# Kernel optimization log

Hardware: AMD Instinct MI355X
Metric: run time of the kernel (lower is better)

Reference implementation:

```python
import jax, jax.numpy as jnp
import numpy as np
from jax import lax

B, DIM, H, W = 32, 256, 64, 64
DS = DIM // 4          # dim_split = 64
MLP_H = int(DIM * 2.0)  # mlp_ratio = 2.0
AK = 11                 # att_kernel
EPS = 1e-5


def conv(x, w, b=None, padding=(0, 0), dilation=1, groups=1, stride=1):
    y = lax.conv_general_dilated(
        x, w, (stride, stride),
        [(padding[0], padding[0]), (padding[1], padding[1])],
        rhs_dilation=(dilation, dilation),
        dimension_numbers=('NCHW', 'OIHW', 'NCHW'),
        feature_group_count=groups)
    if b is not None:
        y = y + b[None, :, None, None]
    return y


def bn(x):
    # BatchNorm2d, training-mode batch stats, affine at default init (gamma=1, beta=0)
    m = x.mean(axis=(0, 2, 3), keepdims=True)
    v = ((x - m) ** 2).mean(axis=(0, 2, 3), keepdims=True)
    return (x - m) * lax.rsqrt(v + EPS)


def maxpool2x2(x):
    b, c, h, w = x.shape
    xw = x.reshape(b, c, h // 2, 2, w // 2, 2).transpose(0, 1, 2, 4, 3, 5).reshape(b, c, h // 2, w // 2, 4)
    return xw.max(axis=-1), jnp.argmax(xw, axis=-1)


def maxunpool2x2(y, idx):
    b, c, h, w = y.shape
    oh = jax.nn.one_hot(idx, 4, dtype=y.dtype)  # scatter back into 2x2 window argmax slot
    out = (y[..., None] * oh).reshape(b, c, h, w, 2, 2).transpose(0, 1, 2, 4, 3, 5)
    return out.reshape(b, c, 2 * h, 2 * w)


def maxpool3(x):
    return lax.reduce_window(x, -jnp.inf, lax.max, (1, 1, 3, 3), (1, 1, 1, 1),
                             [(0, 0), (0, 0), (1, 1), (1, 1)])


def blurpool(x):
    # antialiased_cnns.BlurPool(C, stride=3): filt_size=4, reflect pad (1,2)
    f = jnp.array([1., 3., 3., 1.], dtype=x.dtype)
    k = f[:, None] * f[None, :]
    k = k / k.sum()
    c = x.shape[1]
    wgt = jnp.broadcast_to(k[None, None], (c, 1, 4, 4))
    xp = jnp.pad(x, ((0, 0), (0, 0), (1, 2), (1, 2)), mode='reflect')
    return lax.conv_general_dilated(xp, wgt, (3, 3), [(0, 0), (0, 0)],
                                    dimension_numbers=('NCHW', 'OIHW', 'NCHW'),
                                    feature_group_count=c)


def h_tf(x):
    b, c, hh, ww = x.shape
    x = jnp.pad(x, ((0, 0), (0, 0), (0, 0), (0, ww)))
    x = x.reshape(b, c, -1)[..., :-ww]
    return x.reshape(b, c, hh, 2 * ww - 1)


def inv_h_tf(x):
    b, c, hh, _ = x.shape
    x = x.reshape(b, c, -1)
    x = jnp.pad(x, ((0, 0), (0, 0), (0, hh)))
    return x.reshape(b, c, hh, 2 * hh)[..., :hh]


def v_tf(x):
    return h_tf(x.transpose(0, 1, 3, 2)).transpose(0, 1, 3, 2)


def inv_v_tf(x):
    return inv_h_tf(x.transpose(0, 1, 3, 2)).transpose(0, 1, 3, 2)


def ga12(x, p1w, p1b, c0w, c0b, spw, spb, c1w, c1b, c2w, c2b, cw, cb, sqw, sqb, p2w, p2b):
    xp, idx = maxpool2x2(x)
    c = xp.shape[1]
    h = jax.nn.relu(conv(xp, p1w, p1b))
    a1 = conv(h, c0w, c0b, padding=(2, 2), groups=c)                 # depthwise 5x5
    a2 = conv(a1, spw, spb, padding=(9, 9), dilation=3, groups=c)    # depthwise 7x7 dil3
    a1s = conv(a1, c1w, c1b)
    a2s = conv(a2, c2w, c2b)
    comb = jnp.concatenate([a1s, a2s], axis=1)
    agg = jnp.concatenate([comb.mean(axis=1, keepdims=True),
                           comb.max(axis=1, keepdims=True)], axis=1)
    sig = jax.nn.sigmoid(conv(agg, sqw, sqb, padding=(3, 3)))
    attn = conv(a1s * sig[:, 0:1] + a2s * sig[:, 1:2], cw, cb)
    h = conv(h * attn, p2w, p2b)
    return maxunpool2x2(h, idx)


def setup_inputs() -> dict:
    key = jax.random.key(0)
    ks = jax.random.split(key, 32)
    r = lambda i, shape: jax.random.normal(ks[i], shape, jnp.float32) * 0.05
    return {
        'x': jax.random.normal(ks[0], (B, DIM, H, W), jnp.float32),
        'pa_w1': r(1, (4 * DS, DS, 1, 1)),
        'pa_w2': r(2, (DS, 4 * DS, 1, 1)),
        'la_w': r(3, (DS, DS, 3, 3)),
        'mra_h1': r(4, (DS, 1, AK, 3)),
        'mra_v1': r(5, (DS, 1, 3, AK)),
        'mra_h2': r(6, (DS, 1, AK, 3)),
        'mra_v2': r(7, (DS, 1, 3, AK)),
        'g_proj1_w': r(8, (DS, DS, 1, 1)), 'g_proj1_b': r(9, (DS,)),
        'g_conv0_w': r(10, (DS, 1, 5, 5)), 'g_conv0_b': r(11, (DS,)),
        'g_sp_w': r(12, (DS, 1, 7, 7)), 'g_sp_b': r(13, (DS,)),
        'g_c1_w': r(14, (DS // 2, DS, 1, 1)), 'g_c1_b': r(15, (DS // 2,)),
        'g_c2_w': r(16, (DS // 2, DS, 1, 1)), 'g_c2_b': r(17, (DS // 2,)),
        'g_c_w': r(18, (DS, DS // 2, 1, 1)), 'g_c_b': r(19, (DS,)),
        'g_sq_w': r(20, (2, 2, 7, 7)), 'g_sq_b': r(21, (2,)),
        'g_proj2_w': r(22, (DS, DS, 1, 1)), 'g_proj2_b': r(23, (DS,)),
        'mlp_w1': r(24, (MLP_H, DIM, 1, 1)),
        'mlp_w2': r(25, (DIM, MLP_H, 1, 1)),
    }


def reference(x, pa_w1, pa_w2, la_w, mra_h1, mra_v1, mra_h2, mra_v2,
              g_proj1_w, g_proj1_b, g_conv0_w, g_conv0_b, g_sp_w, g_sp_b,
              g_c1_w, g_c1_b, g_c2_w, g_c2_b, g_c_w, g_c_b,
              g_sq_w, g_sq_b, g_proj2_w, g_proj2_b, mlp_w1, mlp_w2):
    x1, x2, x3, x4 = jnp.split(x, 4, axis=1)
    # PA: pixel attention (1x1 expand -> BN -> ReLU -> 1x1) sigmoid gate
    xa1 = x1 * jax.nn.sigmoid(conv(jax.nn.relu(bn(conv(x1, pa_w1))), pa_w2))
    # LA: 3x3 conv -> BN -> ReLU
    xa2 = jax.nn.relu(bn(conv(x2, la_w, padding=(1, 1))))
    # MRA: maxpool3x3 -> blurpool(stride3) -> 4 strip depthwise convs (+diag shear) -> BN -> sigmoid -> nearest upsample gate
    xm = blurpool(maxpool3(x3))
    ph, pv = (AK // 2, 1), (1, AK // 2)
    xh1 = conv(xm, mra_h1, padding=ph, groups=DS)
    xw1 = conv(xm, mra_v1, padding=pv, groups=DS)
    xh2 = inv_h_tf(conv(h_tf(xm), mra_h2, padding=ph, groups=DS))
    xw2 = inv_v_tf(conv(v_tf(xm), mra_v2, padding=pv, groups=DS))
    gate = jax.nn.sigmoid(bn(xh1 + xw1 + xh2 + xw2))
    hs, ws = gate.shape[-2:]
    ri = (jnp.arange(H) * hs) // H   # torch F.interpolate mode='nearest' index rule
    ci = (jnp.arange(W) * ws) // W
    xa3 = x3 * gate[:, :, ri][:, :, :, ci]
    # D_GA (stage==2): maxpool -> GA12 -> BN -> maxunpool
    x4p, idx1 = maxpool2x2(x4)
    xg = ga12(x4p, g_proj1_w, g_proj1_b, g_conv0_w, g_conv0_b, g_sp_w, g_sp_b,
              g_c1_w, g_c1_b, g_c2_w, g_c2_b, g_c_w, g_c_b, g_sq_w, g_sq_b,
              g_proj2_w, g_proj2_b)
    xa4 = maxunpool2x2(bn(xg), idx1)
    x_att = jnp.concatenate([xa1, xa2, xa3, xa4], axis=1)
    # residual MLP (drop_path=0 -> identity)
    return x + conv(jax.nn.relu(bn(conv(x_att, mlp_w1))), mlp_w2)
```

## Files before the change

### kernel.cpp

```cpp
#include <hip/hip_runtime.h>
#include <hip/hip_bf16.h>
#include <math.h>

typedef __hip_bfloat16 bf16;
typedef __attribute__((ext_vector_type(4))) float f32x4;
typedef __attribute__((ext_vector_type(8))) short s16x8;
typedef __attribute__((ext_vector_type(4))) short s16x4;

static __device__ __forceinline__ float bits2f(short s){ return __uint_as_float(((unsigned)(unsigned short)s)<<16); }
static __device__ __forceinline__ short bfbits(float f){ bf16 h = __float2bfloat16(f); return *reinterpret_cast<short*>(&h); }
static __device__ __forceinline__ float ldf(float v){ return v; }
static __device__ __forceinline__ float sigm(float v){ return 1.f/(1.f+__expf(-v)); }

#define P_IMG 4096

#define GLDS16(SRC, DST) __builtin_amdgcn_global_load_lds( \
    (__attribute__((address_space(1))) void*)(SRC), \
    (__attribute__((address_space(3))) void*)(DST), 16, 0, 0)

namespace {
constexpr long long XATT_OFF = 0;
constexpr long long BIG_OFF  = 67108864;
constexpr long long MISC     = 134217728;
constexpr long long XM_OFF   = MISC;
constexpr long long MSUM_OFF = MISC + 3964928;
constexpr long long SH_OFF   = MISC + 7929856;
constexpr long long SH2_OFF  = MISC + 15679488;
constexpr long long X4P_OFF  = MISC + 23429120;
constexpr long long IDX1_OFF = MISC + 31817728;
constexpr long long XP_OFF   = MISC + 40206336;
constexpr long long IDX2_OFF = MISC + 42303488;
constexpr long long HBUF_OFF = MISC + 44400640;
constexpr long long A1_OFF   = MISC + 46497792;
constexpr long long A2_OFF   = MISC + 48594944;
constexpr long long A1S_OFF  = MISC + 50692096;
constexpr long long A2S_OFF  = MISC + 51740672;
constexpr long long AGG_OFF  = MISC + 52789248;
constexpr long long SIG_OFF  = MISC + 52854784;
constexpr long long ATTN_OFF = MISC + 52920320;
constexpr long long H2_OFF   = MISC + 55017472;
constexpr long long XG_OFF   = MISC + 57114624;
constexpr long long P33_OFF  = 201326592;
constexpr long long STATS_OFF= 234881024;
constexpr long long WS_NEED  = 234897408;
constexpr long long XPM_OFF  = MISC;
constexpr long long YLA_OFF  = MISC + 33554432;
}

__global__ __launch_bounds__(256) void zero_out_k(float* __restrict__ o, int n){
    int i = blockIdx.x*256 + threadIdx.x;
    if (i < n) o[i] = 0.f;
}

__global__ __launch_bounds__(256) void packw_k(const float* __restrict__ W, short* __restrict__ Wp,
                                               int kshift, int OT16)
{
    int i = blockIdx.x*256 + threadIdx.x;
    int o = i >> kshift;
    int k = i & ((1<<kshift)-1);
    long dest = (((((long)(k>>6)*2 + ((k>>5)&1))*OT16 + (o>>4))*4 + ((k>>3)&3))*16 + (o&15))*8 + (k&7);
    Wp[dest] = bfbits(W[i]);
}

__global__ __launch_bounds__(256) void packw_la_k(const float* __restrict__ W, short* __restrict__ Wp)
{
    int i = blockIdx.x*256 + threadIdx.x;
    int o = i / 576, k = i - o*576;
    int tap = k >> 6, c = k & 63;
    long dest = (((((long)(k>>6)*2 + ((k>>5)&1))*4 + (o>>4))*4 + ((k>>3)&3))*16 + (o&15))*8 + (k&7);
    Wp[dest] = bfbits(W[(o*64 + c)*9 + tap]);
}

__global__ __launch_bounds__(256) void xpose_pm_k(const float* __restrict__ x, short* __restrict__ xpm)
{
    int i = blockIdx.x*256 + threadIdx.x;
    int px = i & 4095, og = (i >> 12) & 15, b = i >> 16;
    s16x8 ov;
    #pragma unroll
    for (int j=0;j<8;j++)
        ov[j] = bfbits(x[((long)b*256 + og*8 + j)*P_IMG + px]);
    *(s16x8*)&xpm[((long)b*P_IMG + px)*128 + og*8] = ov;
}

__global__ __launch_bounds__(256) void convmfma_dma_k(
    const short* __restrict__ in, int inCtot, int inOff,
    const short* __restrict__ Wp, int K, int OT16,
    short* __restrict__ out, int outC)
{
    __shared__ __align__(16) short sB[64*64];
    const int tid = threadIdx.x;
    const int b = blockIdx.z;
    const int Mbase = blockIdx.y * 64;
    const int pxBase = blockIdx.x * 64;
    const int lane = tid & 63, w = tid >> 6;
    const int n16 = lane & 15, q = lane >> 4;
    const int wm = w >> 1, wn = w & 1;
    const int otBase = (Mbase>>4) + wm*2;

    f32x4 zero = {0.f,0.f,0.f,0.f};
    f32x4 acc[2][2];
    acc[0][0]=zero; acc[0][1]=zero; acc[1][0]=zero; acc[1][1]=zero;

    const int drow_lo = lane >> 3;
    const int chunk = lane & 7;

    for (int kb = 0; kb < K; kb += 64){
        __syncthreads();
        #pragma unroll
        for (int s = 0; s < 2; s++){
            int seg = w*2 + s;
            int row = seg*8 + drow_lo;
            int kg = chunk ^ (row & 7);
            const short* src = in + ((long)b*P_IMG + pxBase + row)*inCtot + inOff + kb + kg*8;
            GLDS16(src, (char*)sB + seg*1024);
        }
        __syncthreads();
        #pragma unroll
        for (int kk = 0; kk < 2; kk++){
            s16x8 afr[2], bfr[2];
            #pragma unroll
            for (int mt=0; mt<2; mt++)
                afr[mt] = *(const s16x8*)(Wp + ((((long)(kb>>6)*2 + kk)*OT16 + otBase + mt)*64 + lane)*8);
            #pragma unroll
            for (int nt=0; nt<2; nt++){
                int n = wn*32 + nt*16 + n16;
                int g = (kk*4 + q) ^ (n & 7);
                bfr[nt] = *(const s16x8*)&sB[n*64 + (g<<3)];
            }
            #pragma unroll
            for (int mt=0; mt<2; mt++)
                #pragma unroll
                for (int nt=0; nt<2; nt++)
                    acc[mt][nt] = __builtin_amdgcn_mfma_f32_16x16x32_bf16(afr[mt], bfr[nt], acc[mt][nt], 0, 0, 0);
        }
    }

    #pragma unroll
    for (int mt=0; mt<2; mt++){
        #pragma unroll
        for (int nt=0; nt<2; nt++){
            int px = pxBase + wn*32 + nt*16 + n16;
            int o0 = Mbase + wm*32 + mt*16 + q*4;
            s16x4 ov;
            #pragma unroll
            for (int r=0; r<4; r++) ov[r] = bfbits(acc[mt][nt][r]);
            *(s16x4*)&out[((long)b*P_IMG + px)*outC + o0] = ov;
        }
    }
}

__global__ __launch_bounds__(256) void la_mfma_k(
    const short* __restrict__ xpm,
    const short* __restrict__ Wp,
    short* __restrict__ y)
{
    __shared__ __align__(16) short sB[64*64];
    const int tid = threadIdx.x;
    const int b = blockIdx.z;
    const int hRow = blockIdx.x;
    const int pxBase = hRow*64;
    const int lane = tid & 63, w = tid >> 6;
    const int n16 = lane & 15, q = lane >> 4;
    const int wm = w >> 1, wn = w & 1;
    const int otBase = wm*2;

    f32x4 zero = {0.f,0.f,0.f,0.f};
    f32x4 acc[2][2];
    acc[0][0]=zero; acc[0][1]=zero; acc[1][0]=zero; acc[1][1]=zero;

    const int srow = tid >> 3, schunk = tid & 7;

    for (int tap = 0; tap < 9; tap++){
        const int hh = hRow + (tap/3) - 1;
        const int dw = (tap%3) - 1;
        const bool hok = (unsigned)hh < 64u;
        s16x8 stg[2];
        #pragma unroll
        for (int it = 0; it < 2; it++){
            int row = it*32 + srow;
            int ww = row + dw;
            int kg = schunk ^ (row & 7);
            s16x8 v = {0,0,0,0,0,0,0,0};
            if (hok && (unsigned)ww < 64u)
                v = *(const s16x8*)(xpm + ((long)b*P_IMG + hh*64 + ww)*128 + 64 + kg*8);
            stg[it] = v;
        }
        __syncthreads();
        *(s16x8*)&sB[srow*64 + schunk*8]      = stg[0];
        *(s16x8*)&sB[(32+srow)*64 + schunk*8] = stg[1];
        __syncthreads();
        #pragma unroll
        for (int kk = 0; kk < 2; kk++){
            s16x8 afr[2], bfr[2];
            #pragma unroll
            for (int mt=0; mt<2; mt++)
                afr[mt] = *(const s16x8*)(Wp + ((((long)tap*2 + kk)*4 + otBase + mt)*64 + lane)*8);
            #pragma unroll
            for (int nt=0; nt<2; nt++){
                int n = wn*32 + nt*16 + n16;
                int g = (kk*4 + q) ^ (n & 7);
                bfr[nt] = *(const s16x8*)&sB[n*64 + (g<<3)];
            }
            #pragma unroll
            for (int mt=0; mt<2; mt++)
                #pragma unroll
                for (int nt=0; nt<2; nt++)
                    acc[mt][nt] = __builtin_amdgcn_mfma_f32_16x16x32_bf16(afr[mt], bfr[nt], acc[mt][nt], 0, 0, 0);
        }
    }

    #pragma unroll
    for (int mt=0; mt<2; mt++){
        #pragma unroll
        for (int nt=0; nt<2; nt++){
            int px = pxBase + wn*32 + nt*16 + n16;
            int o0 = wm*32 + mt*16 + q*4;
            s16x4 ov;
            #pragma unroll
            for (int r=0; r<4; r++) ov[r] = bfbits(acc[mt][nt][r]);
            *(s16x4*)&y[((long)b*P_IMG + px)*64 + o0] = ov;
        }
    }
}

template<int EPI, typename TOUT>
__global__ __launch_bounds__(256) void convmfma_reg_k(
    const short* __restrict__ in, int inCtot, int inOff,
    const float2* __restrict__ stats,
    const short* __restrict__ Wp, int K, int OT16,
    TOUT* __restrict__ out, int outC, int outOff,
    const float* __restrict__ aux, int auxC, int auxOff)
{
    __shared__ __align__(16) short sB[64*64];
    const int tid = threadIdx.x;
    const int b = blockIdx.z;
    const int Mbase = blockIdx.y * 64;
    const int pxBase = blockIdx.x * 64;
    const int lane = tid & 63, w = tid >> 6;
    const int n16 = lane & 15, q = lane >> 4;
    const int wm = w >> 1, wn = w & 1;
    const int otBase = (Mbase>>4) + wm*2;

    f32x4 zero = {0.f,0.f,0.f,0.f};
    f32x4 acc[2][2];
    acc[0][0]=zero; acc[0][1]=zero; acc[1][0]=zero; acc[1][1]=zero;

    const int srow = tid >> 3, schunk = tid & 7;
    const int skg = schunk ^ (srow & 7);

    for (int kb = 0; kb < K; kb += 64){
        const f32x4* sp = (const f32x4*)(stats + kb + skg*8);
        f32x4 p0 = sp[0], p1 = sp[1], p2 = sp[2], p3 = sp[3];
        float mm[8] = {p0[0],p0[2],p1[0],p1[2],p2[0],p2[2],p3[0],p3[2]};
        float iv[8] = {p0[1],p0[3],p1[1],p1[3],p2[1],p2[3],p3[1],p3[3]};
        s16x8 stg[2];
        #pragma unroll
        for (int it = 0; it < 2; it++){
            int row = it*32 + srow;
            s16x8 rv = *(const s16x8*)(in + ((long)b*P_IMG + pxBase + row)*inCtot + inOff + kb + skg*8);
            s16x8 ov;
            #pragma unroll
            for (int j=0;j<8;j++){
                float f = bits2f(rv[j]);
                f = (f - mm[j])*iv[j];
                f = fmaxf(f, 0.f);
                ov[j] = bfbits(f);
            }
            stg[it] = ov;
        }
        __syncthreads();
        *(s16x8*)&sB[srow*64 + schunk*8]      = stg[0];
        *(s16x8*)&sB[(32+srow)*64 + schunk*8] = stg[1];
        __syncthreads();
        #pragma unroll
        for (int kk = 0; kk < 2; kk++){
            s16x8 afr[2], bfr[2];
            #pragma unroll
            for (int mt=0; mt<2; mt++)
                afr[mt] = *(const s16x8*)(Wp + ((((long)(kb>>6)*2 + kk)*OT16 + otBase + mt)*64 + lane)*8);
            #pragma unroll
            for (int nt=0; nt<2; nt++){
                int n = wn*32 + nt*16 + n16;
                int g = (kk*4 + q) ^ (n & 7);
                bfr[nt] = *(const s16x8*)&sB[n*64 + (g<<3)];
            }
            #pragma unroll
            for (int mt=0; mt<2; mt++)
                #pragma unroll
                for (int nt=0; nt<2; nt++)
                    acc[mt][nt] = __builtin_amdgcn_mfma_f32_16x16x32_bf16(afr[mt], bfr[nt], acc[mt][nt], 0, 0, 0);
        }
    }

    #pragma unroll
    for (int mt=0; mt<2; mt++){
        #pragma unroll
        for (int nt=0; nt<2; nt++){
            int px = pxBase + wn*32 + nt*16 + n16;
            int o0 = Mbase + wm*32 + mt*16 + q*4;
            if constexpr (EPI == 1){
                s16x4 ov;
                #pragma unroll
                for (int r=0; r<4; r++){
                    float av = aux[((long)b*auxC + auxOff + o0 + r)*P_IMG + px];
                    ov[r] = bfbits(av * sigm(acc[mt][nt][r]));
                }
                *(s16x4*)&(((short*)out)[((long)b*P_IMG + px)*outC + outOff + o0]) = ov;
            } else {
                #pragma unroll
                for (int r=0; r<4; r++){
                    int o = o0 + r;
                    float av = aux[((long)b*auxC + auxOff + o)*P_IMG + px];
                    out[((long)b*outC + outOff + o)*P_IMG + px] = av + acc[mt][nt][r];
                }
            }
        }
    }
}

template<int C>
__global__ __launch_bounds__(256) void bnstats_pm_k(const short* __restrict__ in, float* __restrict__ sums)
{
    constexpr int CH8 = C/8;
    constexpr int PL  = 256/CH8;
    __shared__ float accs[2*C];
    const int t = threadIdx.x;
    for (int i=t;i<2*C;i+=256) accs[i]=0.f;
    __syncthreads();
    const int chunk = t & (CH8-1), pl = t / CH8;
    const int b = blockIdx.y;
    float s[8], s2[8];
    #pragma unroll
    for (int j=0;j<8;j++){ s[j]=0.f; s2[j]=0.f; }
    for (int px = blockIdx.x*256 + pl; px < (blockIdx.x+1)*256; px += PL){
        s16x8 v = *(const s16x8*)&in[((long)b*P_IMG + px)*C + chunk*8];
        #pragma unroll
        for (int j=0;j<8;j++){
            float f = bits2f(v[j]);
            s[j] += f; s2[j] = fmaf(f,f,s2[j]);
        }
    }
    #pragma unroll
    for (int j=0;j<8;j++){
        atomicAdd(&accs[(chunk*8+j)*2],   s[j]);
        atomicAdd(&accs[(chunk*8+j)*2+1], s2[j]);
    }
    __syncthreads();
    for (int i=t;i<2*C;i+=256) atomicAdd(&sums[i], accs[i]);
}

template<typename T>
__global__ __launch_bounds__(256) void bnstats_k(const T* __restrict__ in, int Ctot, int cOff, int Pn,
                                                 float* __restrict__ sums)
{
    const int c = blockIdx.x;
    float s=0.f, s2=0.f;
    for (int b=0;b<32;b++){
        const T* qp = in + ((long)b*Ctot + cOff + c)*Pn;
        for (int p = blockIdx.y*256 + threadIdx.x; p < Pn; p += gridDim.y*256){
            float v = ldf(qp[p]);
            s += v; s2 = fmaf(v,v,s2);
        }
    }
    __shared__ float r1[256], r2[256];
    r1[threadIdx.x]=s; r2[threadIdx.x]=s2;
    __syncthreads();
    for (int k=128;k>0;k>>=1){
        if (threadIdx.x<k){ r1[threadIdx.x]+=r1[threadIdx.x+k]; r2[threadIdx.x]+=r2[threadIdx.x+k]; }
        __syncthreads();
    }
    if (threadIdx.x==0){ atomicAdd(&sums[2*c], r1[0]); atomicAdd(&sums[2*c+1], r2[0]); }
}

__global__ __launch_bounds__(256) void bnfin_k(const float* __restrict__ sums, float2* __restrict__ minv,
                                               int C, float invN)
{
    int c = blockIdx.x*256 + threadIdx.x;
    if (c < C){
        float m = sums[2*c]*invN;
        float var = sums[2*c+1]*invN - m*m;
        minv[c] = make_float2(m, 1.f/sqrtf(var + 1e-5f));
    }
}

__global__ __launch_bounds__(256) void la_post_pm_k(const short* __restrict__ y, const float2* __restrict__ minv,
                                                    short* __restrict__ xatt)
{
    int i = blockIdx.x*256 + threadIdx.x;
    int px = i & 4095, og = (i >> 12) & 7, b = i >> 15;
    s16x8 yv = *(const s16x8*)&y[((long)b*P_IMG + px)*64 + og*8];
    s16x8 ov;
    #pragma unroll
    for (int j=0;j<8;j++){
        float2 st = minv[og*8 + j];
        float v = (bits2f(yv[j]) - st.x)*st.y;
        ov[j] = bfbits(fmaxf(v, 0.f));
    }
    *(s16x8*)&xatt[((long)b*P_IMG + px)*256 + 64 + og*8] = ov;
}

__global__ __launch_bounds__(256) void mp3_k(const float* __restrict__ x, float* __restrict__ mp){
    int i = blockIdx.x*256 + threadIdx.x;
    int b = i >> 18, c = (i >> 12) & 63, p = i & 4095;
    int h = p >> 6, wc = p & 63;
    const float* xb = x + ((long)b*256 + 128 + c)*P_IMG;
    float m = -3.4e38f;
    #pragma unroll
    for (int dh=-1; dh<=1; dh++){
        int hh = h+dh; if ((unsigned)hh>=64u) continue;
        #pragma unroll
        for (int dw=-1; dw<=1; dw++){
            int ww = wc+dw; if ((unsigned)ww>=64u) continue;
            m = fmaxf(m, xb[hh*64+ww]);
        }
    }
    mp[i] = m;
}

__global__ __launch_bounds__(256) void blur_k(const float* __restrict__ mp, float* __restrict__ xm){
    int idx = blockIdx.x*256 + threadIdx.x;
    int oj = idx % 22; int t = idx / 22; int oi = t % 22; int bc = t / 22;
    const float* mb = mp + (long)bc * P_IMG;
    const float fw[4] = {1.f,3.f,3.f,1.f};
    float s = 0.f;
    #pragma unroll
    for (int u=0;u<4;u++){
        int r = 3*oi - 1 + u;
        r = r < 0 ? -r : (r > 63 ? 126 - r : r);
        float rs = 0.f;
        #pragma unroll
        for (int v=0; v<4; v++){
            int qq = 3*oj - 1 + v;
            qq = qq < 0 ? -qq : (qq > 63 ? 126 - qq : qq);
            rs = fmaf(fw[v], mb[r*64+qq], rs);
        }
        s = fmaf(fw[u], rs, s);
    }
    xm[idx] = s * (1.f/64.f);
}

__global__ __launch_bounds__(256) void strips_k(const float* __restrict__ xm, const float* __restrict__ wh1,
                                                const float* __restrict__ wv1, float* __restrict__ msum)
{
    int idx = blockIdx.x*256 + threadIdx.x;
    int j = idx % 22; int t = idx / 22; int i = t % 22; int bc = t / 22; int c = bc & 63;
    const float* xb = xm + (long)bc*484;
    float s = 0.f;
    #pragma unroll
    for (int u=0;u<11;u++){
        int ii = i + u - 5; if ((unsigned)ii >= 22u) continue;
        #pragma unroll
        for (int v=0;v<3;v++){
            int jj = j + v - 1; if ((unsigned)jj >= 22u) continue;
            s = fmaf(wh1[c*33 + u*3 + v], xb[ii*22+jj], s);
        }
    }
    #pragma unroll
    for (int u=0;u<3;u++){
        int ii = i + u - 1; if ((unsigned)ii >= 22u) continue;
        #pragma unroll
        for (int v=0;v<11;v++){
            int jj = j + v - 5; if ((unsigned)jj >= 22u) continue;
            s = fmaf(wv1[c*33 + u*11 + v], xb[ii*22+jj], s);
        }
    }
    msum[idx] = s;
}

__global__ __launch_bounds__(256) void shearh_k(const float* __restrict__ xm, float* __restrict__ sh){
    int idx = blockIdx.x*256 + threadIdx.x;
    int j = idx % 43; int t = idx / 43; int i = t % 22; int bc = t / 22;
    int f = i*43 + j; int r = f / 44; int q = f - 44*r;
    sh[idx] = (q < 22) ? xm[(long)bc*484 + r*22 + q] : 0.f;
}

__global__ __launch_bounds__(256) void shconvh_k(const float* __restrict__ sh, const float* __restrict__ w2,
                                                 float* __restrict__ sh2)
{
    int idx = blockIdx.x*256 + threadIdx.x;
    int j = idx % 43; int t = idx / 43; int i = t % 22; int bc = t / 22; int c = bc & 63;
    const float* sb = sh + (long)bc*946;
    float s = 0.f;
    #pragma unroll
    for (int u=0;u<11;u++){
        int ii = i + u - 5; if ((unsigned)ii >= 22u) continue;
        #pragma unroll
        for (int v=0;v<3;v++){
            int jj = j + v - 1; if ((unsigned)jj >= 43u) continue;
            s = fmaf(w2[c*33 + u*3 + v], sb[ii*43+jj], s);
        }
    }
    sh2[idx] = s;
}

__global__ __launch_bounds__(256) void shaddh_k(const float* __restrict__ sh2, float* __restrict__ msum){
    int idx = blockIdx.x*256 + threadIdx.x;
    int j = idx % 22; int t = idx / 22; int i = t % 22; int bc = t / 22;
    int f = i*44 + j; int r = f / 43; int q = f - 43*r;
    msum[idx] += sh2[(long)bc*946 + r*43 + q];
}

__global__ __launch_bounds__(256) void shearv_k(const float* __restrict__ xm, float* __restrict__ sv){
    int idx = blockIdx.x*256 + threadIdx.x;
    int j = idx % 22; int t = idx / 22; int i = t % 43; int bc = t / 43;
    int g = j*43 + i; int r = g / 44; int q = g - 44*r;
    sv[idx] = (q < 22) ? xm[(long)bc*484 + q*22 + r] : 0.f;
}

__global__ __launch_bounds__(256) void shconvv_k(const float* __restrict__ sv, const float* __restrict__ wv2,
                                                 float* __restrict__ sv2)
{
    int idx = blockIdx.x*256 + threadIdx.x;
    int j = idx % 22; int t = idx / 22; int i = t % 43; int bc = t / 43; int c = bc & 63;
    const float* sb = sv + (long)bc*946;
    float s = 0.f;
    #pragma unroll
    for (int u=0;u<3;u++){
        int ii = i + u - 1; if ((unsigned)ii >= 43u) continue;
        #pragma unroll
        for (int v=0;v<11;v++){
            int jj = j + v - 5; if ((unsigned)jj >= 22u) continue;
            s = fmaf(wv2[c*33 + u*11 + v], sb[ii*22+jj], s);
        }
    }
    sv2[idx] = s;
}

__global__ __launch_bounds__(256) void shaddv_k(const float* __restrict__ sv2, float* __restrict__ msum){
    int idx = blockIdx.x*256 + threadIdx.x;
    int xcol = idx % 22; int t = idx / 22; int y = t % 22; int bc = t / 22;
    int g = xcol*44 + y; int r = g / 43; int q = g - 43*r;
    msum[idx] += sv2[(long)bc*946 + q*22 + r];
}

__global__ __launch_bounds__(256) void mra_gate_pm_k(const float* __restrict__ x, const float* __restrict__ msum,
                                                     const float2* __restrict__ minv, short* __restrict__ xatt)
{
    int i = blockIdx.x*256 + threadIdx.x;
    int px = i & 4095, og = (i >> 12) & 7, b = i >> 15;
    int h = px >> 6, wcol = px & 63;
    int ri = (h*22) >> 6, ci = (wcol*22) >> 6;
    s16x8 ov;
    #pragma unroll
    for (int j=0;j<8;j++){
        int c = og*8 + j;
        float g = msum[((long)b*64 + c)*484 + ri*22 + ci];
        float2 st = minv[c];
        g = sigm((g - st.x)*st.y);
        float xv = x[((long)b*256 + 128 + c)*P_IMG + px];
        ov[j] = bfbits(xv * g);
    }
    *(s16x8*)&xatt[((long)b*P_IMG + px)*256 + 128 + og*8] = ov;
}

__global__ __launch_bounds__(256) void pool1_k(const float* __restrict__ x, float* __restrict__ x4p,
                                               int* __restrict__ idx1)
{
    int i = blockIdx.x*256 + threadIdx.x;
    int b = i >> 16, c = (i >> 10) & 63, s = i & 1023;
    int y = s >> 5, xc = s & 31;
    const float* xb = x + ((long)b*256 + 192 + c)*P_IMG;
    float v00 = xb[(2*y)*64 + 2*xc];
    float v01 = xb[(2*y)*64 + 2*xc + 1];
    float v10 = xb[(2*y+1)*64 + 2*xc];
    float v11 = xb[(2*y+1)*64 + 2*xc + 1];
    float best = v00; int bi = 0;
    if (v01 > best){ best = v01; bi = 1; }
    if (v10 > best){ best = v10; bi = 2; }
    if (v11 > best){ best = v11; bi = 3; }
    x4p[i] = best; idx1[i] = bi;
}

__global__ __launch_bounds__(256) void pool2_k(const float* __restrict__ x4p, float* __restrict__ xp,
                                               int* __restrict__ idx2)
{
    int i = blockIdx.x*256 + threadIdx.x;
    int b = i >> 14, c = (i >> 8) & 63, s = i & 255;
    int y = s >> 4, xc = s & 15;
    const float* xb = x4p + ((long)b*64 + c)*1024;
    float v00 = xb[(2*y)*32 + 2*xc];
    float v01 = xb[(2*y)*32 + 2*xc + 1];
    float v10 = xb[(2*y+1)*32 + 2*xc];
    float v11 = xb[(2*y+1)*32 + 2*xc + 1];
    float best = v00; int bi = 0;
    if (v01 > best){ best = v01; bi = 1; }
    if (v10 > best){ best = v10; bi = 2; }
    if (v11 > best){ best = v11; bi = 3; }
    xp[i] = best; idx2[i] = bi;
}

__global__ __launch_bounds__(256) void ga_proj_k(const float* __restrict__ in, const float* __restrict__ mul,
                                                 const float* __restrict__ w, const float* __restrict__ bias,
                                                 float* __restrict__ out, int Cout, int relu)
{
    int s = threadIdx.x, og = blockIdx.x, b = blockIdx.y;
    float acc[8];
    #pragma unroll
    for (int j=0;j<8;j++) acc[j]=0.f;
    for (int c=0;c<64;c++){
        float v = in[((long)b*64 + c)*256 + s];
        if (mul) v *= mul[((long)b*64 + c)*256 + s];
        #pragma unroll
        for (int j=0;j<8;j++) acc[j] = fmaf(v, w[(og*8 + j)*64 + c], acc[j]);
    }
    #pragma unroll
    for (int j=0;j<8;j++){
        int o = og*8 + j;
        float val = acc[j] + bias[o];
        if (relu) val = fmaxf(val, 0.f);
        out[((long)b*Cout + o)*256 + s] = val;
    }
}

__global__ __launch_bounds__(256) void ga_dw5_k(const float* __restrict__ h, const float* __restrict__ w,
                                                const float* __restrict__ bias, float* __restrict__ a1)
{
    int i = blockIdx.x*256 + threadIdx.x;
    int b = i >> 14, c = (i >> 8) & 63, s = i & 255;
    int y = s >> 4, x = s & 15;
    const float* hb = h + ((long)b*64 + c)*256;
    float acc = bias[c];
    #pragma unroll
    for (int u=0;u<5;u++){
        int yy = y + u - 2; if ((unsigned)yy >= 16u) continue;
        #pragma unroll
        for (int v=0;v<5;v++){
            int xx = x + v - 2; if ((unsigned)xx >= 16u) continue;
            acc = fmaf(w[c*25 + u*5 + v], hb[yy*16 + xx], acc);
        }
    }
    a1[i] = acc;
}

__global__ __launch_bounds__(256) void ga_dw7_k(const float* __restrict__ a1, const float* __restrict__ w,
                                                const float* __restrict__ bias, float* __restrict__ a2)
{
    int i = blockIdx.x*256 + threadIdx.x;
    int b = i >> 14, c = (i >> 8) & 63, s = i & 255;
    int y = s >> 4, x = s & 15;
    const float* ab = a1 + ((long)b*64 + c)*256;
    float acc = bias[c];
    #pragma unroll
    for (int u=0;u<7;u++){
        int yy = y + 3*(u-3); if ((unsigned)yy >= 16u) continue;
        #pragma unroll
        for (int v=0;v<7;v++){
            int xx = x + 3*(v-3); if ((unsigned)xx >= 16u) continue;
            acc = fmaf(w[c*49 + u*7 + v], ab[yy*16 + xx], acc);
        }
    }
    a2[i] = acc;
}

__global__ __launch_bounds__(256) void ga_agg_k(const float* __restrict__ a1s, const float* __restrict__ a2s,
                                                float* __restrict__ agg)
{
    int i = blockIdx.x*256 + threadIdx.x;
    int b = i >> 8, s = i & 255;
    float sum = 0.f, mx = -3.4e38f;
    for (int c=0;c<32;c++){
        float v = a1s[((long)b*32 + c)*256 + s];
        sum += v; mx = fmaxf(mx, v);
    }
    for (int c=0;c<32;c++){
        float v = a2s[((long)b*32 + c)*256 + s];
        sum += v; mx = fmaxf(mx, v);
    }
    agg[((long)b*2 + 0)*256 + s] = sum * (1.f/64.f);
    agg[((long)b*2 + 1)*256 + s] = mx;
}

__global__ __launch_bounds__(256) void ga_sq_k(const float* __restrict__ agg, const float* __restrict__ w,
                                               const float* __restrict__ bias, float* __restrict__ sig)
{
    int i = blockIdx.x*256 + threadIdx.x;
    int b = i >> 9, o = (i >> 8) & 1, s = i & 255;
    int y = s >> 4, x = s & 15;
    float acc = bias[o];
    for (int ic=0; ic<2; ic++){
        const float* ab = agg + ((long)b*2 + ic)*256;
        #pragma unroll
        for (int u=0;u<7;u++){
            int yy = y + u - 3; if ((unsigned)yy >= 16u) continue;
            #pragma unroll
            for (int v=0;v<7;v++){
                int xx = x + v - 3; if ((unsigned)xx >= 16u) continue;
                acc = fmaf(w[((o*2 + ic)*7 + u)*7 + v], ab[yy*16 + xx], acc);
            }
        }
    }
    sig[i] = sigm(acc);
}

__global__ __launch_bounds__(256) void ga_attn_k(const float* __restrict__ a1s, const float* __restrict__ a2s,
                                                 const float* __restrict__ sig, const float* __restrict__ w,
                                                 const float* __restrict__ bias, float* __restrict__ attn)
{
    int s = threadIdx.x, og = blockIdx.x, b = blockIdx.y;
    float s0 = sig[((long)b*2 + 0)*256 + s];
    float s1 = sig[((long)b*2 + 1)*256 + s];
    float acc[8];
    #pragma unroll
    for (int j=0;j<8;j++) acc[j]=0.f;
    for (int c=0;c<32;c++){
        float v = a1s[((long)b*32 + c)*256 + s]*s0 + a2s[((long)b*32 + c)*256 + s]*s1;
        #pragma unroll
        for (int j=0;j<8;j++) acc[j] = fmaf(v, w[(og*8 + j)*32 + c], acc[j]);
    }
    #pragma unroll
    for (int j=0;j<8;j++){
        int o = og*8 + j;
        attn[((long)b*64 + o)*256 + s] = acc[j] + bias[o];
    }
}

__global__ __launch_bounds__(256) void ga_unpool1_k(const float* __restrict__ h2, const int* __restrict__ idx2,
                                                    float* __restrict__ xg)
{
    int i = blockIdx.x*256 + threadIdx.x;
    int b = i >> 16, c = (i >> 10) & 63, s = i & 1023;
    int Y = s >> 5, X = s & 31;
    int slot = ((Y & 1) << 1) | (X & 1);
    long pi = ((long)b*64 + c)*256 + (Y >> 1)*16 + (X >> 1);
    xg[i] = (idx2[pi] == slot) ? h2[pi] : 0.f;
}

__global__ __launch_bounds__(256) void ga_out_pm_k(const float* __restrict__ xg, const int* __restrict__ idx1,
                                                   const float2* __restrict__ minv, short* __restrict__ xatt)
{
    int i = blockIdx.x*256 + threadIdx.x;
    int px = i & 4095, og = (i >> 12) & 7, b = i >> 15;
    int hh = px >> 6, ww = px & 63;
    int slot = ((hh & 1) << 1) | (ww & 1);
    s16x8 ov;
    #pragma unroll
    for (int j=0;j<8;j++){
        int c = og*8 + j;
        long pi = ((long)b*64 + c)*1024 + (hh >> 1)*32 + (ww >> 1);
        float v = 0.f;
        if (idx1[pi] == slot){
            float2 st = minv[c];
            v = (xg[pi] - st.x)*st.y;
        }
        ov[j] = bfbits(v);
    }
    *(s16x8*)&xatt[((long)b*P_IMG + px)*256 + 192 + og*8] = ov;
}

extern "C" void kernel_launch(void* const* d_in, const int* in_sizes, int n_in,
                              void* d_out, int out_size, void* d_ws, size_t ws_size,
                              hipStream_t stream)
{
    const float* x      = (const float*)d_in[0];
    const float* pa_w1  = (const float*)d_in[1];
    const float* pa_w2  = (const float*)d_in[2];
    const float* la_w   = (const float*)d_in[3];
    const float* mra_h1 = (const float*)d_in[4];
    const float* mra_v1 = (const float*)d_in[5];
    const float* mra_h2 = (const float*)d_in[6];
    const float* mra_v2 = (const float*)d_in[7];
    const float* g_p1w  = (const float*)d_in[8];
    const float* g_p1b  = (const float*)d_in[9];
    const float* g_c0w  = (const float*)d_in[10];
    const float* g_c0b  = (const float*)d_in[11];
    const float* g_spw  = (const float*)d_in[12];
    const float* g_spb  = (const float*)d_in[13];
    const float* g_c1w  = (const float*)d_in[14];
    const float* g_c1b  = (const float*)d_in[15];
    const float* g_c2w  = (const float*)d_in[16];
    const float* g_c2b  = (const float*)d_in[17];
    const float* g_cw   = (const float*)d_in[18];
    const float* g_cb   = (const float*)d_in[19];
    const float* g_sqw  = (const float*)d_in[20];
    const float* g_sqb  = (const float*)d_in[21];
    const float* g_p2w  = (const float*)d_in[22];
    const float* g_p2b  = (const float*)d_in[23];
    const float* mlp_w1 = (const float*)d_in[24];
    const float* mlp_w2 = (const float*)d_in[25];
    float* outp = (float*)d_out;
    char* ws = (char*)d_ws;

    if (ws_size < (size_t)WS_NEED){
        zero_out_k<<<(out_size + 255)/256, 256, 0, stream>>>(outp, out_size);
        return;
    }

    short* xatt = (short*)(ws + XATT_OFF);
    short* tbuf = (short*)(ws + BIG_OFF);
    short* xpm  = (short*)(ws + XPM_OFF);
    short* yla  = (short*)(ws + YLA_OFF);
    float* xm   = (float*)(ws + XM_OFF);
    float* msum = (float*)(ws + MSUM_OFF);
    float* sh   = (float*)(ws + SH_OFF);
    float* sh2  = (float*)(ws + SH2_OFF);
    float* x4p  = (float*)(ws + X4P_OFF);
    int*   idx1 = (int*)(ws + IDX1_OFF);
    float* xp   = (float*)(ws + XP_OFF);
    int*   idx2 = (int*)(ws + IDX2_OFF);
    float* hbuf = (float*)(ws + HBUF_OFF);
    float* a1   = (float*)(ws + A1_OFF);
    float* a2   = (float*)(ws + A2_OFF);
    float* a1s  = (float*)(ws + A1S_OFF);
    float* a2s  = (float*)(ws + A2S_OFF);
    float* agg  = (float*)(ws + AGG_OFF);
    float* sig  = (float*)(ws + SIG_OFF);
    float* attn = (float*)(ws + ATTN_OFF);
    float* h2   = (float*)(ws + H2_OFF);
    float* xg   = (float*)(ws + XG_OFF);
    float* p33  = (float*)(ws + P33_OFF);
    float* raw  = (float*)(ws + STATS_OFF);
    float*  raw_pa  = raw;
    float*  raw_la  = raw + 512;
    float*  raw_mra = raw + 640;
    float*  raw_ga  = raw + 768;
    float*  raw_mlp = raw + 896;
    float2* mv_pa   = (float2*)(raw + 1920);
    float2* mv_la   = mv_pa + 256;
    float2* mv_mra  = mv_la + 64;
    float2* mv_ga   = mv_mra + 64;
    float2* mv_mlp  = mv_ga + 64;

    hipMemsetAsync(raw, 0, 1920*sizeof(float), stream);

    short* wp_pa1 = (short*)(ws + P33_OFF);
    short* wp_pa2 = wp_pa1 + 256*64;
    short* wp_la  = wp_pa2 + 64*256;
    packw_k<<<64,256,0,stream>>>(pa_w1, wp_pa1, 6, 16);
    packw_k<<<64,256,0,stream>>>(pa_w2, wp_pa2, 8, 4);
    packw_la_k<<<144,256,0,stream>>>(la_w, wp_la);

    xpose_pm_k<<<8192,256,0,stream>>>(x, xpm);

    convmfma_dma_k<<<dim3(64,4,32),256,0,stream>>>(xpm,128,0, wp_pa1,64,16, tbuf,256);
    bnstats_pm_k<256><<<dim3(16,32),256,0,stream>>>(tbuf, raw_pa);
    bnfin_k<<<1,256,0,stream>>>(raw_pa, mv_pa, 256, 1.f/131072.f);
    convmfma_reg_k<1,short><<<dim3(64,1,32),256,0,stream>>>(tbuf,256,0, mv_pa, wp_pa2,256,4,
                                                            xatt,256,0, x,256,0);

    la_mfma_k<<<dim3(64,1,32),256,0,stream>>>(xpm, wp_la, yla);
    bnstats_pm_k<64><<<dim3(16,32),256,0,stream>>>(yla, raw_la);
    bnfin_k<<<1,256,0,stream>>>(raw_la, mv_la, 64, 1.f/131072.f);
    la_post_pm_k<<<4096,256,0,stream>>>(yla, mv_la, xatt);

    mp3_k<<<32768,256,0,stream>>>(x, p33);
    blur_k<<<3872,256,0,stream>>>(p33, xm);
    strips_k<<<3872,256,0,stream>>>(xm, mra_h1, mra_v1, msum);
    shearh_k<<<7568,256,0,stream>>>(xm, sh);
    shconvh_k<<<7568,256,0,stream>>>(sh, mra_h2, sh2);
    shaddh_k<<<3872,256,0,stream>>>(sh2, msum);
    shearv_k<<<7568,256,0,stream>>>(xm, sh);
    shconvv_k<<<7568,256,0,stream>>>(sh, mra_v2, sh2);
    shaddv_k<<<3872,256,0,stream>>>(sh2, msum);
    bnstats_k<float><<<dim3(64,2),256,0,stream>>>(msum,64,0,484, raw_mra);
    bnfin_k<<<1,256,0,stream>>>(raw_mra, mv_mra, 64, 1.f/15488.f);
    mra_gate_pm_k<<<4096,256,0,stream>>>(x, msum, mv_mra, xatt);

    pool1_k<<<8192,256,0,stream>>>(x, x4p, idx1);
    pool2_k<<<2048,256,0,stream>>>(x4p, xp, idx2);
    ga_proj_k<<<dim3(8,32),256,0,stream>>>(xp, nullptr, g_p1w, g_p1b, hbuf, 64, 1);
    ga_dw5_k<<<2048,256,0,stream>>>(hbuf, g_c0w, g_c0b, a1);
    ga_dw7_k<<<2048,256,0,stream>>>(a1, g_spw, g_spb, a2);
    ga_proj_k<<<dim3(4,32),256,0,stream>>>(a1, nullptr, g_c1w, g_c1b, a1s, 32, 0);
    ga_proj_k<<<dim3(4,32),256,0,stream>>>(a2, nullptr, g_c2w, g_c2b, a2s, 32, 0);
    ga_agg_k<<<32,256,0,stream>>>(a1s, a2s, agg);
    ga_sq_k<<<64,256,0,stream>>>(agg, g_sqw, g_sqb, sig);
    ga_attn_k<<<dim3(8,32),256,0,stream>>>(a1s, a2s, sig, g_cw, g_cb, attn);
    ga_proj_k<<<dim3(8,32),256,0,stream>>>(hbuf, attn, g_p2w, g_p2b, h2, 64, 0);
    ga_unpool1_k<<<8192,256,0,stream>>>(h2, idx2, xg);
    bnstats_k<float><<<dim3(64,4),256,0,stream>>>(xg,64,0,1024, raw_ga);
    bnfin_k<<<1,256,0,stream>>>(raw_ga, mv_ga, 64, 1.f/32768.f);
    ga_out_pm_k<<<4096,256,0,stream>>>(xg, idx1, mv_ga, xatt);

    short* wm1 = (short*)(ws + P33_OFF);
    short* wm2 = wm1 + 512*256;
    packw_k<<<512,256,0,stream>>>(mlp_w1, wm1, 8, 32);
    packw_k<<<512,256,0,stream>>>(mlp_w2, wm2, 9, 16);
    convmfma_dma_k<<<dim3(64,8,32),256,0,stream>>>(xatt,256,0, wm1,256,32, tbuf,512);
    bnstats_pm_k<512><<<dim3(16,32),256,0,stream>>>(tbuf, raw_mlp);
    bnfin_k<<<2,256,0,stream>>>(raw_mlp, mv_mlp, 512, 1.f/131072.f);
    convmfma_reg_k<2,float><<<dim3(64,4,32),256,0,stream>>>(tbuf,512,0, mv_mlp, wm2,512,16,
                                                            outp,256,0, x,256,0);
}
```

Measured before the change: 1.048 ms.

## Widen GEMM output tiles and fuse MRA shear convolutions into one kernel

The MFMA conv kernels get a template parameter for the number of 16-row output tiles per wave, and the PA1, MLP1 and MLP2 GEMMs now use 128-channel blocks. Each staged activation tile is then reused across twice as many output channels, which halves redundant input loads and block count. Separately, the MRA diagonal shear transform, strip conv and add-back kernels are folded into one kernel that computes the sheared convolutions by index arithmetic directly from xm. This drops six launches and the intermediate buffers, at the cost of more accumulator registers and heavier integer index math per thread.

```diff
diff --git a/kernel.cpp b/kernel.cpp
--- a/kernel.cpp
+++ b/kernel.cpp
@@ -82,6 +82,7 @@
     *(s16x8*)&xpm[((long)b*P_IMG + px)*128 + og*8] = ov;
 }
 
+template<int MT>
 __global__ __launch_bounds__(256) void convmfma_dma_k(
     const short* __restrict__ in, int inCtot, int inOff,
     const short* __restrict__ Wp, int K, int OT16,
@@ -90,16 +91,17 @@
     __shared__ __align__(16) short sB[64*64];
     const int tid = threadIdx.x;
     const int b = blockIdx.z;
-    const int Mbase = blockIdx.y * 64;
+    const int Mbase = blockIdx.y * (32*MT);
     const int pxBase = blockIdx.x * 64;
     const int lane = tid & 63, w = tid >> 6;
     const int n16 = lane & 15, q = lane >> 4;
     const int wm = w >> 1, wn = w & 1;
-    const int otBase = (Mbase>>4) + wm*2;
+    const int otBase = (Mbase>>4) + wm*MT;
 
     f32x4 zero = {0.f,0.f,0.f,0.f};
-    f32x4 acc[2][2];
-    acc[0][0]=zero; acc[0][1]=zero; acc[1][0]=zero; acc[1][1]=zero;
+    f32x4 acc[MT][2];
+    #pragma unroll
+    for (int mt=0;mt<MT;mt++){ acc[mt][0]=zero; acc[mt][1]=zero; }
 
     const int drow_lo = lane >> 3;
     const int chunk = lane & 7;
@@ -117,9 +119,9 @@
         __syncthreads();
         #pragma unroll
         for (int kk = 0; kk < 2; kk++){
-            s16x8 afr[2], bfr[2];
-            #pragma unroll
-            for (int mt=0; mt<2; mt++)
+            s16x8 afr[MT], bfr[2];
+            #pragma unroll
+            for (int mt=0; mt<MT; mt++)
                 afr[mt] = *(const s16x8*)(Wp + ((((long)(kb>>6)*2 + kk)*OT16 + otBase + mt)*64 + lane)*8);
             #pragma unroll
             for (int nt=0; nt<2; nt++){
@@ -128,7 +130,7 @@
                 bfr[nt] = *(const s16x8*)&sB[n*64 + (g<<3)];
             }
             #pragma unroll
-            for (int mt=0; mt<2; mt++)
+            for (int mt=0; mt<MT; mt++)
                 #pragma unroll
                 for (int nt=0; nt<2; nt++)
                     acc[mt][nt] = __builtin_amdgcn_mfma_f32_16x16x32_bf16(afr[mt], bfr[nt], acc[mt][nt], 0, 0, 0);
@@ -136,11 +138,11 @@
     }
 
     #pragma unroll
-    for (int mt=0; mt<2; mt++){
+    for (int mt=0; mt<MT; mt++){
         #pragma unroll
         for (int nt=0; nt<2; nt++){
             int px = pxBase + wn*32 + nt*16 + n16;
-            int o0 = Mbase + wm*32 + mt*16 + q*4;
+            int o0 = Mbase + wm*(MT*16) + mt*16 + q*4;
             s16x4 ov;
             #pragma unroll
             for (int r=0; r<4; r++) ov[r] = bfbits(acc[mt][nt][r]);
@@ -223,7 +225,7 @@
     }
 }
 
-template<int EPI, typename TOUT>
+template<int EPI, typename TOUT, int MT>
 __global__ __launch_bounds__(256) void convmfma_reg_k(
     const short* __restrict__ in, int inCtot, int inOff,
     const float2* __restrict__ stats,
@@ -234,16 +236,17 @@
     __shared__ __align__(16) short sB[64*64];
     const int tid = threadIdx.x;
     const int b = blockIdx.z;
-    const int Mbase = blockIdx.y * 64;
+    const int Mbase = blockIdx.y * (32*MT);
     const int pxBase = blockIdx.x * 64;
     const int lane = tid & 63, w = tid >> 6;
     const int n16 = lane & 15, q = lane >> 4;
     const int wm = w >> 1, wn = w & 1;
-    const int otBase = (Mbase>>4) + wm*2;
+    const int otBase = (Mbase>>4) + wm*MT;
 
     f32x4 zero = {0.f,0.f,0.f,0.f};
-    f32x4 acc[2][2];
-    acc[0][0]=zero; acc[0][1]=zero; acc[1][0]=zero; acc[1][1]=zero;
+    f32x4 acc[MT][2];
+    #pragma unroll
+    for (int mt=0;mt<MT;mt++){ acc[mt][0]=zero; acc[mt][1]=zero; }
 
     const int srow = tid >> 3, schunk = tid & 7;
     const int skg = schunk ^ (srow & 7);
@@ -274,9 +277,9 @@
         __syncthreads();
         #pragma unroll
         for (int kk = 0; kk < 2; kk++){
-            s16x8 afr[2], bfr[2];
-            #pragma unroll
-            for (int mt=0; mt<2; mt++)
+            s16x8 afr[MT], bfr[2];
+            #pragma unroll
+            for (int mt=0; mt<MT; mt++)
                 afr[mt] = *(const s16x8*)(Wp + ((((long)(kb>>6)*2 + kk)*OT16 + otBase + mt)*64 + lane)*8);
             #pragma unroll
             for (int nt=0; nt<2; nt++){
@@ -285,7 +288,7 @@
                 bfr[nt] = *(const s16x8*)&sB[n*64 + (g<<3)];
             }
             #pragma unroll
-            for (int mt=0; mt<2; mt++)
+            for (int mt=0; mt<MT; mt++)
                 #pragma unroll
                 for (int nt=0; nt<2; nt++)
                     acc[mt][nt] = __builtin_amdgcn_mfma_f32_16x16x32_bf16(afr[mt], bfr[nt], acc[mt][nt], 0, 0, 0);
@@ -293,11 +296,11 @@
     }
 
     #pragma unroll
-    for (int mt=0; mt<2; mt++){
+    for (int mt=0; mt<MT; mt++){
         #pragma unroll
         for (int nt=0; nt<2; nt++){
             int px = pxBase + wn*32 + nt*16 + n16;
-            int o0 = Mbase + wm*32 + mt*16 + q*4;
+            int o0 = Mbase + wm*(MT*16) + mt*16 + q*4;
             if constexpr (EPI == 1){
                 s16x4 ov;
                 #pragma unroll
@@ -439,8 +442,10 @@
     xm[idx] = s * (1.f/64.f);
 }
 
-__global__ __launch_bounds__(256) void strips_k(const float* __restrict__ xm, const float* __restrict__ wh1,
-                                                const float* __restrict__ wv1, float* __restrict__ msum)
+__global__ __launch_bounds__(256) void mra_conv_k(const float* __restrict__ xm,
+                                                  const float* __restrict__ wh1, const float* __restrict__ wv1,
+                                                  const float* __restrict__ wh2, const float* __restrict__ wv2,
+                                                  float* __restrict__ msum)
 {
     int idx = blockIdx.x*256 + threadIdx.x;
     int j = idx % 22; int t = idx / 22; int i = t % 22; int bc = t / 22; int c = bc & 63;
@@ -464,73 +469,33 @@
             s = fmaf(wv1[c*33 + u*11 + v], xb[ii*22+jj], s);
         }
     }
+    {
+        int f = i*44 + j; int r = f/43; int q = f - 43*r;
+        #pragma unroll
+        for (int u=0;u<11;u++){
+            int a = r + u - 5; if ((unsigned)a >= 22u) continue;
+            #pragma unroll
+            for (int v=0;v<3;v++){
+                int bcol = q + v - 1; if ((unsigned)bcol >= 43u) continue;
+                int g = a*43 + bcol; int rr = g/44; int qq = g - 44*rr;
+                if (qq < 22) s = fmaf(wh2[c*33 + u*3 + v], xb[rr*22+qq], s);
+            }
+        }
+    }
+    {
+        int g = j*44 + i; int r = g/43; int q = g - 43*r;
+        #pragma unroll
+        for (int u=0;u<3;u++){
+            int a = q + u - 1; if ((unsigned)a >= 43u) continue;
+            #pragma unroll
+            for (int v=0;v<11;v++){
+                int bcol = r + v - 5; if ((unsigned)bcol >= 22u) continue;
+                int g2 = bcol*43 + a; int rr = g2/44; int qq = g2 - 44*rr;
+                if (qq < 22) s = fmaf(wv2[c*33 + u*11 + v], xb[qq*22+rr], s);
+            }
+        }
+    }
     msum[idx] = s;
-}
-
-__global__ __launch_bounds__(256) void shearh_k(const float* __restrict__ xm, float* __restrict__ sh){
-    int idx = blockIdx.x*256 + threadIdx.x;
-    int j = idx % 43; int t = idx / 43; int i = t % 22; int bc = t / 22;
-    int f = i*43 + j; int r = f / 44; int q = f - 44*r;
-    sh[idx] = (q < 22) ? xm[(long)bc*484 + r*22 + q] : 0.f;
-}
-
-__global__ __launch_bounds__(256) void shconvh_k(const float* __restrict__ sh, const float* __restrict__ w2,
-                                                 float* __restrict__ sh2)
-{
-    int idx = blockIdx.x*256 + threadIdx.x;
-    int j = idx % 43; int t = idx / 43; int i = t % 22; int bc = t / 22; int c = bc & 63;
-    const float* sb = sh + (long)bc*946;
-    float s = 0.f;
-    #pragma unroll
-    for (int u=0;u<11;u++){
-        int ii = i + u - 5; if ((unsigned)ii >= 22u) continue;
-        #pragma unroll
-        for (int v=0;v<3;v++){
-            int jj = j + v - 1; if ((unsigned)jj >= 43u) continue;
-            s = fmaf(w2[c*33 + u*3 + v], sb[ii*43+jj], s);
-        }
-    }
-    sh2[idx] = s;
-}
-
-__global__ __launch_bounds__(256) void shaddh_k(const float* __restrict__ sh2, float* __restrict__ msum){
-    int idx = blockIdx.x*256 + threadIdx.x;
-    int j = idx % 22; int t = idx / 22; int i = t % 22; int bc = t / 22;
-    int f = i*44 + j; int r = f / 43; int q = f - 43*r;
-    msum[idx] += sh2[(long)bc*946 + r*43 + q];
-}
-
-__global__ __launch_bounds__(256) void shearv_k(const float* __restrict__ xm, float* __restrict__ sv){
-    int idx = blockIdx.x*256 + threadIdx.x;
-    int j = idx % 22; int t = idx / 22; int i = t % 43; int bc = t / 43;
-    int g = j*43 + i; int r = g / 44; int q = g - 44*r;
-    sv[idx] = (q < 22) ? xm[(long)bc*484 + q*22 + r] : 0.f;
-}
-
-__global__ __launch_bounds__(256) void shconvv_k(const float* __restrict__ sv, const float* __restrict__ wv2,
-                                                 float* __restrict__ sv2)
-{
-    int idx = blockIdx.x*256 + threadIdx.x;
-    int j = idx % 22; int t = idx / 22; int i = t % 43; int bc = t / 43; int c = bc & 63;
-    const float* sb = sv + (long)bc*946;
-    float s = 0.f;
-    #pragma unroll
-    for (int u=0;u<3;u++){
-        int ii = i + u - 1; if ((unsigned)ii >= 43u) continue;
-        #pragma unroll
-        for (int v=0;v<11;v++){
-            int jj = j + v - 5; if ((unsigned)jj >= 22u) continue;
-            s = fmaf(wv2[c*33 + u*11 + v], sb[ii*22+jj], s);
-        }
-    }
-    sv2[idx] = s;
-}
-
-__global__ __launch_bounds__(256) void shaddv_k(const float* __restrict__ sv2, float* __restrict__ msum){
-    int idx = blockIdx.x*256 + threadIdx.x;
-    int xcol = idx % 22; int t = idx / 22; int y = t % 22; int bc = t / 22;
-    int g = xcol*44 + y; int r = g / 43; int q = g - 43*r;
-    msum[idx] += sv2[(long)bc*946 + q*22 + r];
 }
 
 __global__ __launch_bounds__(256) void mra_gate_pm_k(const float* __restrict__ x, const float* __restrict__ msum,
@@ -791,8 +756,6 @@
     short* yla  = (short*)(ws + YLA_OFF);
     float* xm   = (float*)(ws + XM_OFF);
     float* msum = (float*)(ws + MSUM_OFF);
-    float* sh   = (float*)(ws + SH_OFF);
-    float* sh2  = (float*)(ws + SH2_OFF);
     float* x4p  = (float*)(ws + X4P_OFF);
     int*   idx1 = (int*)(ws + IDX1_OFF);
     float* xp   = (float*)(ws + XP_OFF);
@@ -831,11 +794,11 @@
 
     xpose_pm_k<<<8192,256,0,stream>>>(x, xpm);
 
-    convmfma_dma_k<<<dim3(64,4,32),256,0,stream>>>(xpm,128,0, wp_pa1,64,16, tbuf,256);
+    convmfma_dma_k<4><<<dim3(64,2,32),256,0,stream>>>(xpm,128,0, wp_pa1,64,16, tbuf,256);
     bnstats_pm_k<256><<<dim3(16,32),256,0,stream>>>(tbuf, raw_pa);
     bnfin_k<<<1,256,0,stream>>>(raw_pa, mv_pa, 256, 1.f/131072.f);
-    convmfma_reg_k<1,short><<<dim3(64,1,32),256,0,stream>>>(tbuf,256,0, mv_pa, wp_pa2,256,4,
-                                                            xatt,256,0, x,256,0);
+    convmfma_reg_k<1,short,2><<<dim3(64,1,32),256,0,stream>>>(tbuf,256,0, mv_pa, wp_pa2,256,4,
+                                                              xatt,256,0, x,256,0);
 
     la_mfma_k<<<dim3(64,1,32),256,0,stream>>>(xpm, wp_la, yla);
     bnstats_pm_k<64><<<dim3(16,32),256,0,stream>>>(yla, raw_la);
@@ -844,13 +807,7 @@
 
     mp3_k<<<32768,256,0,stream>>>(x, p33);
     blur_k<<<3872,256,0,stream>>>(p33, xm);
-    strips_k<<<3872,256,0,stream>>>(xm, mra_h1, mra_v1, msum);
-    shearh_k<<<7568,256,0,stream>>>(xm, sh);
-    shconvh_k<<<7568,256,0,stream>>>(sh, mra_h2, sh2);
-    shaddh_k<<<3872,256,0,stream>>>(sh2, msum);
-    shearv_k<<<7568,256,0,stream>>>(xm, sh);
-    shconvv_k<<<7568,256,0,stream>>>(sh, mra_v2, sh2);
-    shaddv_k<<<3872,256,0,stream>>>(sh2, msum);
+    mra_conv_k<<<3872,256,0,stream>>>(xm, mra_h1, mra_v1, mra_h2, mra_v2, msum);
     bnstats_k<float><<<dim3(64,2),256,0,stream>>>(msum,64,0,484, raw_mra);
     bnfin_k<<<1,256,0,stream>>>(raw_mra, mv_mra, 64, 1.f/15488.f);
     mra_gate_pm_k<<<4096,256,0,stream>>>(x, msum, mv_mra, xatt);
@@ -875,9 +832,9 @@
     short* wm2 = wm1 + 512*256;
     packw_k<<<512,256,0,stream>>>(mlp_w1, wm1, 8, 32);
     packw_k<<<512,256,0,stream>>>(mlp_w2, wm2, 9, 16);
-    convmfma_dma_k<<<dim3(64,8,32),256,0,stream>>>(xatt,256,0, wm1,256,32, tbuf,512);
+    convmfma_dma_k<4><<<dim3(64,4,32),256,0,stream>>>(xatt,256,0, wm1,256,32, tbuf,512);
     bnstats_pm_k<512><<<dim3(16,32),256,0,stream>>>(tbuf, raw_mlp);
     bnfin_k<<<2,256,0,stream>>>(raw_mlp, mv_mlp, 512, 1.f/131072.f);
-    convmfma_reg_k<2,float><<<dim3(64,4,32),256,0,stream>>>(tbuf,512,0, mv_mlp, wm2,512,16,
-                                                            outp,256,0, x,256,0);
-}
+    convmfma_reg_k<2,float,4><<<dim3(64,2,32),256,0,stream>>>(tbuf,512,0, mv_mlp, wm2,512,16,
+                                                              outp,256,0, x,256,0);
+}
```

After: 980.7 us. -6.5%, faster.
